# Performance work log

Hardware: AMD Instinct MI355X
Metric: run time of the kernel (lower is better)

The kernel has to match this reference:

```python
import jax, jax.numpy as jnp
import numpy as np

B, N, T, H, D = 128, 128, 256, 256, 50


def setup_inputs() -> dict:
    key = jax.random.key(0)
    ks = jax.random.split(key, 13)
    f = lambda k, s, sc=1.0: jax.random.normal(k, s, dtype=jnp.float32) * sc
    return {
        "tokens_h": f(ks[0], (B, N, H)),
        "tokens_c": f(ks[1], (B, N, H)),
        "transitions": jax.random.randint(ks[2], (B, T), 0, 3, dtype=jnp.int32),
        "tlstm_h0": f(ks[3], (B, D)),
        "tlstm_c0": f(ks[4], (B, D)),
        "Wx": f(ks[5], (4, H, D), 0.1),    # [W_i, W_f, W_o, W_u] (W_f unused in fwd, as in source)
        "Ul": f(ks[6], (4, H, H), 0.05),   # [U_il, U_fl, U_ol, U_ul]
        "Ur": f(ks[7], (4, H, H), 0.05),   # [U_ir, U_fr, U_or, U_ur]
        "b": f(ks[8], (4, H), 0.1),        # [b_i, b_f, b_o, b_u]
        "Wih": f(ks[9], (4 * D, 3 * H), 0.05),
        "Whh": f(ks[10], (4 * D, D), 0.1),
        "bih": f(ks[11], (4 * D,), 0.1),
        "bhh": f(ks[12], (4 * D,), 0.1),
    }


def _forward(tokens_h, tokens_c, transitions, tlstm_h0, tlstm_c0,
             Wx, Ul, Ur, b, Wih, Whh, bih, bhh):
    Bb, Nn, Hh = tokens_h.shape
    Tt = transitions.shape[1]
    bidx = jnp.arange(Bb)

    def tree_cell(x, h_r, c_r, h_l, c_l):
        # Faithful to source bugs: i uses W_i, o/f both use W_o, u uses W_u;
        # f_jl == f_jr (identical expressions in source).
        xi = x @ Wx[0].T
        xo = x @ Wx[2].T
        xu = x @ Wx[3].T
        i_j = jax.nn.sigmoid(xi + h_l @ Ul[0].T + h_r @ Ur[0].T + b[0])
        o_j = jax.nn.sigmoid(xo + h_l @ Ul[2].T + h_r @ Ur[2].T + b[2])
        f_j = jax.nn.sigmoid(xo + h_l @ Ul[1].T + h_r @ Ur[1].T + b[1])
        u_j = jnp.tanh(xu + h_l @ Ul[3].T + h_r @ Ur[3].T + b[3])
        c_j = i_j * u_j + f_j * c_l + f_j * c_r
        return o_j * jnp.tanh(c_j), c_j

    stack_h = jnp.zeros((Bb, Tt + 1, Hh), tokens_h.dtype)
    stack_c = jnp.zeros((Bb, Tt + 1, Hh), tokens_h.dtype)
    queue = jnp.zeros((Bb, Tt + 1), jnp.int32)   # backpointer queue (fixed buffer)
    qlen = jnp.zeros((Bb,), jnp.int32)
    bptr = jnp.zeros((Bb,), jnp.int32)

    def step(carry, xs):
        stack_h, stack_c, queue, qlen, bptr, th, tc = carry
        trans_t, t = xs
        mask = trans_t >= 1
        # utils.get_queue_item(q, -1/-2) -> default index 0 (zero stack entry)
        sp1 = jnp.where(qlen >= 1, queue[bidx, jnp.maximum(qlen - 1, 0)], 0)
        sp2 = jnp.where(qlen >= 2, queue[bidx, jnp.maximum(qlen - 2, 0)], 0)
        h1, c1 = stack_h[bidx, sp1], stack_c[bidx, sp1]
        h2, c2 = stack_h[bidx, sp2], stack_c[bidx, sp2]
        bp = jnp.minimum(bptr, Nn - 1)
        bt_h, bt_c = tokens_h[bidx, bp], tokens_c[bidx, bp]
        # tracking LSTMCell, torch gate order (i, f, g, o)
        gates = jnp.concatenate([bt_h, h1, h2], -1) @ Wih.T + bih + th @ Whh.T + bhh
        gi, gf, gg, go = jnp.split(gates, 4, axis=-1)
        tc = jax.nn.sigmoid(gf) * tc + jax.nn.sigmoid(gi) * jnp.tanh(gg)
        th = jax.nn.sigmoid(go) * jnp.tanh(tc)
        # source call order: encoder(x, h_right, c_right, h_left, c_left)
        h_la, c_la = tree_cell(th, h1, h2, c1, c2)          # (x, h_stack1, h_stack2, c_stack1, c_stack2)
        h_ra, c_ra = tree_cell(th, h2, h1, c2, c2)          # (x, h_stack2, h_stack1, c_stack2, c_stack2)
        is0 = (trans_t == 0)[:, None]
        is1 = (trans_t == 1)[:, None]
        new_h = jnp.where(is0, bt_h, jnp.where(is1, h_la, h_ra))
        new_c = jnp.where(is0, bt_c, jnp.where(is1, c_la, c_ra))
        stack_h = stack_h.at[:, t].set(new_h)
        stack_c = stack_c.at[:, t].set(new_c)
        qlen2 = jnp.where(mask, jnp.maximum(qlen - 2, 0), qlen)  # pop two on reduce
        queue = queue.at[bidx, qlen2].set(t)                      # push current timestep
        qlen = qlen2 + 1
        bptr = bptr + (1 - mask.astype(jnp.int32))
        return (stack_h, stack_c, queue, qlen, bptr, th, tc), None

    xs = (transitions.T, jnp.arange(1, Tt + 1, dtype=jnp.int32))
    carry, _ = jax.lax.scan(step, (stack_h, stack_c, queue, qlen, bptr, tlstm_h0, tlstm_c0), xs)
    return carry[0][:, Tt]  # stack[i][-1][0]


def reference(tokens_h, tokens_c, transitions, tlstm_h0, tlstm_c0,
              Wx, Ul, Ur, b, Wih, Whh, bih, bhh):
    return _forward(tokens_h, tokens_c, transitions, tlstm_h0, tlstm_c0,
                    Wx, Ul, Ur, b, Wih, Whh, bih, bhh)
```

## Files before the change

### kernel.cpp

```cpp
#include <hip/hip_runtime.h>
#include <hip/hip_fp16.h>
#include <math.h>
#include <string.h>

#define B_ 128
#define N_ 128
#define T_ 256
#define H_ 256
#define D_ 50

#define TREE_K8 72
#define TRK_K8  104

#define OFF_SH   0u
#define OFF_SC   8421376u
#define OFF_PW   16842752u
#define OFF_WTRK 17137664u
#define OFF_BCOL 17220864u
#define OFF_BTRK 17221888u
#define OFF_FLAG 17222088u
#define OFF_IDX  17287624u

__device__ __forceinline__ float sigf(float x) { return 1.0f / (1.0f + expf(-x)); }

__device__ __forceinline__ float2 h2f(unsigned u) {
    __half2 h;
    memcpy(&h, &u, 4);
    return __half22float2(h);
}

__device__ __forceinline__ float aload(const float* p) {
    int v = __hip_atomic_load((const int*)p, __ATOMIC_RELAXED, __HIP_MEMORY_SCOPE_AGENT);
    return __int_as_float(v);
}
__device__ __forceinline__ void astore(float* p, float x) {
    __hip_atomic_store((int*)p, __float_as_int(x), __ATOMIC_RELAXED, __HIP_MEMORY_SCOPE_AGENT);
}

__global__ void sim_idx(const int* __restrict__ trans, int* __restrict__ idx) {
    int b = blockIdx.x * blockDim.x + threadIdx.x;
    if (b >= B_) return;
    int queue[T_ + 1];
    int qlen = 0, bptr = 0;
    for (int st = 0; st < T_; ++st) {
        int tr = trans[b * T_ + st];
        int mask = (tr >= 1);
        int sp1 = (qlen >= 1) ? queue[qlen - 1] : 0;
        int sp2 = (qlen >= 2) ? queue[qlen - 2] : 0;
        int bp = bptr < (N_ - 1) ? bptr : (N_ - 1);
        int o = (b * T_ + st) * 3;
        idx[o] = sp1; idx[o + 1] = sp2; idx[o + 2] = bp;
        int qlen2 = mask ? (qlen - 2 > 0 ? qlen - 2 : 0) : qlen;
        queue[qlen2] = st + 1;
        qlen = qlen2 + 1;
        bptr += mask ? 0 : 1;
    }
}

__global__ void pack_tree(const float* __restrict__ Ul, const float* __restrict__ Ur,
                          const float* __restrict__ Wx, uint4* __restrict__ PW) {
    int i = blockIdx.x * blockDim.x + threadIdx.x;
    if (i >= 2 * TREE_K8 * 512) return;
    int hw = i / (TREE_K8 * 512);
    int rem = i % (TREE_K8 * 512);
    int k8 = rem / 512, c = rem % 512;
    int C = hw * 512 + c, j = C >> 2, g = C & 3;
    const int gl[4] = {0, 2, 1, 3};
    const int gx[4] = {0, 2, 2, 3};
    unsigned short hs[8];
    for (int kk = 0; kk < 8; ++kk) {
        int r = k8 * 8 + kk;
        float v;
        if (r < 256)      v = Ul[(gl[g] * H_ + j) * H_ + r];
        else if (r < 512) v = Ur[(gl[g] * H_ + j) * H_ + (r - 256)];
        else if (r < 562) v = Wx[(gx[g] * H_ + j) * D_ + (r - 512)];
        else              v = 0.0f;
        __half h = __float2half(v);
        memcpy(&hs[kk], &h, 2);
    }
    uint4 o;
    o.x = hs[0] | ((unsigned)hs[1] << 16);
    o.y = hs[2] | ((unsigned)hs[3] << 16);
    o.z = hs[4] | ((unsigned)hs[5] << 16);
    o.w = hs[6] | ((unsigned)hs[7] << 16);
    PW[i] = o;
}

__global__ void pack_trk(const float* __restrict__ Wih, const float* __restrict__ Whh,
                         uint4* __restrict__ WT) {
    int i = blockIdx.x * blockDim.x + threadIdx.x;
    if (i >= TRK_K8 * 200) return;
    int k8 = i / 200, d = i % 200;
    unsigned short hs[8];
    for (int kk = 0; kk < 8; ++kk) {
        int r = k8 * 8 + kk;
        float v;
        if (r < 768)      v = Wih[d * 768 + r];
        else if (r < 818) v = Whh[d * 50 + (r - 768)];
        else              v = 0.0f;
        __half h = __float2half(v);
        memcpy(&hs[kk], &h, 2);
    }
    uint4 o;
    o.x = hs[0] | ((unsigned)hs[1] << 16);
    o.y = hs[2] | ((unsigned)hs[3] << 16);
    o.z = hs[4] | ((unsigned)hs[5] << 16);
    o.w = hs[6] | ((unsigned)hs[7] << 16);
    WT[i] = o;
}

__global__ void pack_bias(const float* __restrict__ bias4, const float* __restrict__ bih,
                          const float* __restrict__ bhh,
                          float* __restrict__ bcol, float* __restrict__ btrk) {
    int i = blockIdx.x * blockDim.x + threadIdx.x;
    if (i < 1024) {
        int j = i >> 2, g = i & 3;
        const int gb[4] = {0, 2, 1, 3};
        bcol[i] = bias4[gb[g] * H_ + j];
    } else if (i < 1224) {
        int d = i - 1024;
        btrk[d] = bih[d] + bhh[d];
    }
}

__global__ void init_zero(float* __restrict__ ws) {
    int i = blockIdx.x * blockDim.x + threadIdx.x;
    if (i < B_ * T_ * 2) ((int*)(ws + OFF_FLAG))[i] = 0;
    if (i < B_ * H_) {
        int b = i >> 8, j = i & 255;
        ws[OFF_SH + (size_t)b * (T_ + 1) * H_ + j] = 0.0f;
        ws[OFF_SC + (size_t)b * (T_ + 1) * H_ + j] = 0.0f;
    }
}

__global__ __launch_bounds__(1024, 1)
void trnn_main(const float* __restrict__ tokens_h, const float* __restrict__ tokens_c,
               const int* __restrict__ trans,
               const float* __restrict__ th0, const float* __restrict__ tc0,
               float* __restrict__ ws, const int* __restrict__ idx,
               float* __restrict__ out) {
    const int b   = blockIdx.x & 127;
    const int hw  = blockIdx.x >> 7;
    const int tid = threadIdx.x;

    float* stack_h = ws + OFF_SH + (size_t)b * (T_ + 1) * H_;
    float* stack_c = ws + OFF_SC + (size_t)b * (T_ + 1) * H_;
    const uint4* PW = (const uint4*)(ws + OFF_PW);
    const uint4* WT = (const uint4*)(ws + OFF_WTRK);
    const float* bcol = ws + OFF_BCOL;
    const float* btrk = ws + OFF_BTRK;
    int* flags = (int*)(ws + OFF_FLAG);

    __shared__ __align__(16) float avb[256];
    __shared__ __align__(16) float av1[576], av2[576];
    __shared__ float tc_l[50];
    __shared__ float part_t[8][200];
    __shared__ float part1[8][512], part2[8][512];
    __shared__ float act1[512], act2[512];

    if (tid < 50) {
        tc_l[tid] = tc0[b * D_ + tid];
        float t0 = th0[b * D_ + tid];
        av1[512 + tid] = t0;
        av2[512 + tid] = t0;
    }
    if (tid >= 562 && tid < 576) { av1[tid] = 0.0f; av2[tid] = 0.0f; }
    __syncthreads();

    const float4* av1f4 = (const float4*)av1;
    const float4* av2f4 = (const float4*)av2;
    const float4* avbf4 = (const float4*)avb;

    for (int t = 1; t <= T_; ++t) {
        const int st = t - 1;
        const int i3 = (b * T_ + st) * 3;
        const int sp1 = idx[i3], sp2 = idx[i3 + 1], bp = idx[i3 + 2];

        if (t >= 2) {
            if (tid == 0) {
                int* f = &flags[(b * T_ + (t - 1)) * 2 + (hw ^ 1)];
                while (__hip_atomic_load(f, __ATOMIC_RELAXED, __HIP_MEMORY_SCOPE_AGENT) == 0)
                    __builtin_amdgcn_s_sleep(1);
            }
            __syncthreads();
        }

        {
            const int grp = tid >> 8, lane = tid & 255;
            if (grp == 0) {
                av1[lane] = aload(&stack_c[sp1 * H_ + lane]);
                avb[lane] = tokens_h[((size_t)b * N_ + bp) * H_ + lane];
            } else if (grp == 1) {
                av1[256 + lane] = aload(&stack_h[sp1 * H_ + lane]);
            } else if (grp == 2) {
                av2[lane] = aload(&stack_c[sp2 * H_ + lane]);
            } else {
                av2[256 + lane] = aload(&stack_h[sp2 * H_ + lane]);
            }
        }
        __syncthreads();

        if (tid < 512) {
            const int ks = tid >> 6, dgrp = tid & 63;
            if (dgrp < 50) {
                float acc0 = 0.f, acc1s = 0.f, acc2s = 0.f, acc3 = 0.f;
                for (int i = 0; i < 13; ++i) {
                    const int k8 = ks * 13 + i;
                    const float4* vsrc; int kb;
                    if (k8 < 32)      { vsrc = avbf4;        kb = k8; }
                    else if (k8 < 64) { vsrc = av1f4 + 64;   kb = k8 - 32; }
                    else if (k8 < 96) { vsrc = av2f4 + 64;   kb = k8 - 64; }
                    else              { vsrc = av1f4 + 128;  kb = k8 - 96; }
                    const float4 va = vsrc[kb * 2], vb = vsrc[kb * 2 + 1];
                    const uint4* wrow = WT + k8 * 200 + dgrp;
                    #pragma unroll
                    for (int dg = 0; dg < 4; ++dg) {
                        const uint4 w = wrow[dg * 50];
                        const float2 f0 = h2f(w.x), f1 = h2f(w.y), f2 = h2f(w.z), f3 = h2f(w.w);
                        float s = fmaf(f0.x, va.x, fmaf(f0.y, va.y, fmaf(f1.x, va.z,
                                  fmaf(f1.y, va.w, fmaf(f2.x, vb.x, fmaf(f2.y, vb.y,
                                  fmaf(f3.x, vb.z, f3.y * vb.w)))))));
                        if (dg == 0) acc0 += s;
                        else if (dg == 1) acc1s += s;
                        else if (dg == 2) acc2s += s;
                        else acc3 += s;
                    }
                }
                part_t[ks][dgrp]       = acc0;
                part_t[ks][50 + dgrp]  = acc1s;
                part_t[ks][100 + dgrp] = acc2s;
                part_t[ks][150 + dgrp] = acc3;
            }
        }
        __syncthreads();

        if (tid < 50) {
            float g4[4];
            #pragma unroll
            for (int dg = 0; dg < 4; ++dg) {
                const int d = dg * 50 + tid;
                float s = btrk[d];
                #pragma unroll
                for (int ks = 0; ks < 8; ++ks) s += part_t[ks][d];
                g4[dg] = s;
            }
            float tcv = fmaf(sigf(g4[1]), tc_l[tid], sigf(g4[0]) * tanhf(g4[2]));
            tc_l[tid] = tcv;
            float thv = sigf(g4[3]) * tanhf(tcv);
            av1[512 + tid] = thv;
            av2[512 + tid] = thv;
        }
        __syncthreads();

        {
            const int ks = tid >> 7, colgrp = tid & 127;
            float a1c[4] = {0.f, 0.f, 0.f, 0.f};
            float a2c[4] = {0.f, 0.f, 0.f, 0.f};
            #pragma unroll 3
            for (int i = 0; i < 9; ++i) {
                const int k8 = ks * 9 + i;
                const float4 v1a = av1f4[k8 * 2], v1b = av1f4[k8 * 2 + 1];
                const float4 v2a = av2f4[k8 * 2], v2b = av2f4[k8 * 2 + 1];
                const uint4* wrow = PW + (size_t)(hw * TREE_K8 + k8) * 512 + colgrp;
                #pragma unroll
                for (int cl = 0; cl < 4; ++cl) {
                    const uint4 w = wrow[cl * 128];
                    const float2 f0 = h2f(w.x), f1 = h2f(w.y), f2 = h2f(w.z), f3 = h2f(w.w);
                    float s1 = fmaf(f0.x, v1a.x, fmaf(f0.y, v1a.y, fmaf(f1.x, v1a.z,
                               fmaf(f1.y, v1a.w, fmaf(f2.x, v1b.x, fmaf(f2.y, v1b.y,
                               fmaf(f3.x, v1b.z, f3.y * v1b.w)))))));
                    float s2 = fmaf(f0.x, v2a.x, fmaf(f0.y, v2a.y, fmaf(f1.x, v2a.z,
                               fmaf(f1.y, v2a.w, fmaf(f2.x, v2b.x, fmaf(f2.y, v2b.y,
                               fmaf(f3.x, v2b.z, f3.y * v2b.w)))))));
                    a1c[cl] += s1;
                    a2c[cl] += s2;
                }
            }
            #pragma unroll
            for (int cl = 0; cl < 4; ++cl) {
                part1[ks][cl * 128 + colgrp] = a1c[cl];
                part2[ks][cl * 128 + colgrp] = a2c[cl];
            }
        }
        __syncthreads();

        {
            const int c = tid & 511;
            float s = bcol[hw * 512 + c];
            if (tid < 512) {
                #pragma unroll
                for (int ks = 0; ks < 8; ++ks) s += part1[ks][c];
                act1[c] = ((c & 3) == 3) ? tanhf(s) : sigf(s);
            } else {
                #pragma unroll
                for (int ks = 0; ks < 8; ++ks) s += part2[ks][c];
                act2[c] = ((c & 3) == 3) ? tanhf(s) : sigf(s);
            }
        }
        __syncthreads();

        if (tid < 128) {
            const int jl = tid, j = hw * 128 + jl;
            const float i1 = act1[4 * jl], o1 = act1[4 * jl + 1], f1 = act1[4 * jl + 2], u1 = act1[4 * jl + 3];
            const float i2 = act2[4 * jl], o2 = act2[4 * jl + 1], f2 = act2[4 * jl + 2], u2 = act2[4 * jl + 3];
            const float cc1 = fmaf(i1, u1, f1 * (av2[j] + av2[256 + j]));
            const float cc2 = fmaf(i2, u2, f2 * (av2[j] + av1[256 + j]));
            const float hh1 = o1 * tanhf(cc1);
            const float hh2 = o2 * tanhf(cc2);
            const int tr = trans[b * T_ + st];
            float nh, nc;
            if (tr == 0) {
                nh = avb[j];
                nc = tokens_c[((size_t)b * N_ + bp) * H_ + j];
            } else if (tr == 1) { nh = hh1; nc = cc1; }
            else                { nh = hh2; nc = cc2; }
            astore(&stack_h[t * H_ + j], nh);
            astore(&stack_c[t * H_ + j], nc);
            if (t == T_) out[b * H_ + j] = nh;
        }
        asm volatile("s_waitcnt vmcnt(0)" ::: "memory");
        __syncthreads();
        if (tid == 0 && t < T_) {
            __hip_atomic_store(&flags[(b * T_ + t) * 2 + hw], 1,
                               __ATOMIC_RELEASE, __HIP_MEMORY_SCOPE_AGENT);
        }
    }
}

extern "C" void kernel_launch(void* const* d_in, const int* in_sizes, int n_in,
                              void* d_out, int out_size, void* d_ws, size_t ws_size,
                              hipStream_t stream) {
    (void)in_sizes; (void)n_in; (void)out_size; (void)ws_size;
    const float* tokens_h = (const float*)d_in[0];
    const float* tokens_c = (const float*)d_in[1];
    const int*   trans    = (const int*)d_in[2];
    const float* th0      = (const float*)d_in[3];
    const float* tc0      = (const float*)d_in[4];
    const float* Wx       = (const float*)d_in[5];
    const float* Ul       = (const float*)d_in[6];
    const float* Ur       = (const float*)d_in[7];
    const float* bias4    = (const float*)d_in[8];
    const float* Wih      = (const float*)d_in[9];
    const float* Whh      = (const float*)d_in[10];
    const float* bih      = (const float*)d_in[11];
    const float* bhh      = (const float*)d_in[12];

    float* ws = (float*)d_ws;
    uint4* PW   = (uint4*)(ws + OFF_PW);
    uint4* WT   = (uint4*)(ws + OFF_WTRK);
    float* bcol = ws + OFF_BCOL;
    float* btrk = ws + OFF_BTRK;
    int*   idx  = (int*)(ws + OFF_IDX);

    hipLaunchKernelGGL(init_zero, dim3(256), dim3(256), 0, stream, ws);
    hipLaunchKernelGGL(sim_idx, dim3(1), dim3(128), 0, stream, trans, idx);
    hipLaunchKernelGGL(pack_tree, dim3((2 * TREE_K8 * 512 + 255) / 256), dim3(256), 0, stream,
                       Ul, Ur, Wx, PW);
    hipLaunchKernelGGL(pack_trk, dim3((TRK_K8 * 200 + 255) / 256), dim3(256), 0, stream,
                       Wih, Whh, WT);
    hipLaunchKernelGGL(pack_bias, dim3(5), dim3(256), 0, stream, bias4, bih, bhh, bcol, btrk);
    hipLaunchKernelGGL(trnn_main, dim3(256), dim3(1024), 0, stream,
                       tokens_h, tokens_c, trans, th0, tc0, ws, idx, (float*)d_out);
}
```

Before: 4.084 ms.

## Restructure tree and tracker matvecs with packed fp16 dot2 and register-cached weights

Activation vectors are now packed to fp16 pairs in shared memory, and both matvecs use the fdot2 instruction instead of unpacking to fp32 FMAs. The tracker weights are re-laid out per thread across a 5-way K split, with 12 of 21 chunks held in registers for the whole recurrence. Each tree thread now owns one gate column with a 2-way K split, down from the previous 8-way split, so the shared partial-sum reduction shrinks. tokens_h and tokens_c rows are staged in shared memory at the start of each step. The aim is to cut per-step instruction count, weight reloads from L2, and reduction traffic, at the cost of fp16 rounding of the activations and more register pressure now that launch_bounds no longer fixes one block per SM.

```diff
diff --git a/kernel.cpp b/kernel.cpp
--- a/kernel.cpp
+++ b/kernel.cpp
@@ -1,7 +1,6 @@
 #include <hip/hip_runtime.h>
 #include <hip/hip_fp16.h>
 #include <math.h>
-#include <string.h>
 
 #define B_ 128
 #define N_ 128
@@ -9,24 +8,36 @@
 #define H_ 256
 #define D_ 50
 
-#define TREE_K8 72
-#define TRK_K8  104
+#define TREE_U 72
+#define TRK_U  21
+#define TRK_REGU 12
 
 #define OFF_SH   0u
 #define OFF_SC   8421376u
-#define OFF_PW   16842752u
-#define OFF_WTRK 17137664u
-#define OFF_BCOL 17220864u
-#define OFF_BTRK 17221888u
-#define OFF_FLAG 17222088u
-#define OFF_IDX  17287624u
+#define OFF_PWK  16842752u
+#define OFF_WTK  17137664u
+#define OFF_BCOL 17221664u
+#define OFF_BTRK 17222688u
+#define OFF_FLAG 17222888u
+#define OFF_IDX  17288424u
+
+typedef _Float16 half2v __attribute__((ext_vector_type(2)));
 
 __device__ __forceinline__ float sigf(float x) { return 1.0f / (1.0f + expf(-x)); }
 
-__device__ __forceinline__ float2 h2f(unsigned u) {
-    __half2 h;
-    memcpy(&h, &u, 4);
-    return __half22float2(h);
+__device__ __forceinline__ unsigned packh2(float a, float b) {
+    half2v h = { (_Float16)a, (_Float16)b };
+    return __builtin_bit_cast(unsigned, h);
+}
+
+__device__ __forceinline__ float dot2(unsigned wu, unsigned vu, float acc) {
+#if __has_builtin(__builtin_amdgcn_fdot2)
+    return __builtin_amdgcn_fdot2(__builtin_bit_cast(half2v, wu),
+                                  __builtin_bit_cast(half2v, vu), acc, false);
+#else
+    half2v w = __builtin_bit_cast(half2v, wu), v = __builtin_bit_cast(half2v, vu);
+    return fmaf((float)w.x, (float)v.x, fmaf((float)w.y, (float)v.y, acc));
+#endif
 }
 
 __device__ __forceinline__ float aload(const float* p) {
@@ -60,53 +71,36 @@
 __global__ void pack_tree(const float* __restrict__ Ul, const float* __restrict__ Ur,
                           const float* __restrict__ Wx, uint4* __restrict__ PW) {
     int i = blockIdx.x * blockDim.x + threadIdx.x;
-    if (i >= 2 * TREE_K8 * 512) return;
-    int hw = i / (TREE_K8 * 512);
-    int rem = i % (TREE_K8 * 512);
-    int k8 = rem / 512, c = rem % 512;
-    int C = hw * 512 + c, j = C >> 2, g = C & 3;
+    if (i >= TREE_U * 1024) return;
+    int u = i >> 10, C = i & 1023, j = C >> 2, g = C & 3;
     const int gl[4] = {0, 2, 1, 3};
     const int gx[4] = {0, 2, 2, 3};
-    unsigned short hs[8];
+    float f[8];
     for (int kk = 0; kk < 8; ++kk) {
-        int r = k8 * 8 + kk;
-        float v;
-        if (r < 256)      v = Ul[(gl[g] * H_ + j) * H_ + r];
-        else if (r < 512) v = Ur[(gl[g] * H_ + j) * H_ + (r - 256)];
-        else if (r < 562) v = Wx[(gx[g] * H_ + j) * D_ + (r - 512)];
-        else              v = 0.0f;
-        __half h = __float2half(v);
-        memcpy(&hs[kk], &h, 2);
-    }
-    uint4 o;
-    o.x = hs[0] | ((unsigned)hs[1] << 16);
-    o.y = hs[2] | ((unsigned)hs[3] << 16);
-    o.z = hs[4] | ((unsigned)hs[5] << 16);
-    o.w = hs[6] | ((unsigned)hs[7] << 16);
-    PW[i] = o;
+        int r = u * 8 + kk;
+        if (r < 256)      f[kk] = Ul[(gl[g] * H_ + j) * H_ + r];
+        else if (r < 512) f[kk] = Ur[(gl[g] * H_ + j) * H_ + (r - 256)];
+        else if (r < 562) f[kk] = Wx[(gx[g] * H_ + j) * D_ + (r - 512)];
+        else              f[kk] = 0.0f;
+    }
+    PW[i] = make_uint4(packh2(f[0], f[1]), packh2(f[2], f[3]),
+                       packh2(f[4], f[5]), packh2(f[6], f[7]));
 }
 
 __global__ void pack_trk(const float* __restrict__ Wih, const float* __restrict__ Whh,
                          uint4* __restrict__ WT) {
     int i = blockIdx.x * blockDim.x + threadIdx.x;
-    if (i >= TRK_K8 * 200) return;
-    int k8 = i / 200, d = i % 200;
-    unsigned short hs[8];
+    if (i >= TRK_U * 1000) return;
+    int u = i / 1000, rem = i % 1000, d = rem / 5, ks = rem % 5;
+    float f[8];
     for (int kk = 0; kk < 8; ++kk) {
-        int r = k8 * 8 + kk;
-        float v;
-        if (r < 768)      v = Wih[d * 768 + r];
-        else if (r < 818) v = Whh[d * 50 + (r - 768)];
-        else              v = 0.0f;
-        __half h = __float2half(v);
-        memcpy(&hs[kk], &h, 2);
-    }
-    uint4 o;
-    o.x = hs[0] | ((unsigned)hs[1] << 16);
-    o.y = hs[2] | ((unsigned)hs[3] << 16);
-    o.z = hs[4] | ((unsigned)hs[5] << 16);
-    o.w = hs[6] | ((unsigned)hs[7] << 16);
-    WT[i] = o;
+        int r = ks * 168 + u * 8 + kk;
+        if (r < 768)      f[kk] = Wih[d * 768 + r];
+        else if (r < 818) f[kk] = Whh[d * 50 + (r - 768)];
+        else              f[kk] = 0.0f;
+    }
+    WT[i] = make_uint4(packh2(f[0], f[1]), packh2(f[2], f[3]),
+                       packh2(f[4], f[5]), packh2(f[6], f[7]));
 }
 
 __global__ void pack_bias(const float* __restrict__ bias4, const float* __restrict__ bih,
@@ -133,7 +127,27 @@
     }
 }
 
-__global__ __launch_bounds__(1024, 1)
+template <int S>
+__device__ __forceinline__ void tree_batch(const uint4* __restrict__ wpk, int u0,
+                                           const unsigned* __restrict__ q1,
+                                           const unsigned* __restrict__ q2,
+                                           float& a1, float& a2) {
+    uint4 wb[S];
+#pragma unroll
+    for (int i = 0; i < S; ++i) wb[i] = wpk[(size_t)(u0 + i) << 10];
+#pragma unroll
+    for (int i = 0; i < S; ++i) {
+        const int u = u0 + i;
+        const uint4 v1 = *(const uint4*)(q1 + u * 4);
+        const uint4 v2 = *(const uint4*)(q2 + u * 4);
+        a1 = dot2(wb[i].x, v1.x, a1); a1 = dot2(wb[i].y, v1.y, a1);
+        a1 = dot2(wb[i].z, v1.z, a1); a1 = dot2(wb[i].w, v1.w, a1);
+        a2 = dot2(wb[i].x, v2.x, a2); a2 = dot2(wb[i].y, v2.y, a2);
+        a2 = dot2(wb[i].z, v2.z, a2); a2 = dot2(wb[i].w, v2.w, a2);
+    }
+}
+
+__global__ __launch_bounds__(1024)
 void trnn_main(const float* __restrict__ tokens_h, const float* __restrict__ tokens_c,
                const int* __restrict__ trans,
                const float* __restrict__ th0, const float* __restrict__ tc0,
@@ -145,31 +159,44 @@
 
     float* stack_h = ws + OFF_SH + (size_t)b * (T_ + 1) * H_;
     float* stack_c = ws + OFF_SC + (size_t)b * (T_ + 1) * H_;
-    const uint4* PW = (const uint4*)(ws + OFF_PW);
-    const uint4* WT = (const uint4*)(ws + OFF_WTRK);
+    const uint4* PWK4 = (const uint4*)(ws + OFF_PWK);
+    const uint4* WTK4 = (const uint4*)(ws + OFF_WTK);
     const float* bcol = ws + OFF_BCOL;
     const float* btrk = ws + OFF_BTRK;
     int* flags = (int*)(ws + OFF_FLAG);
 
-    __shared__ __align__(16) float avb[256];
-    __shared__ __align__(16) float av1[576], av2[576];
+    __shared__ __align__(16) unsigned av1[288], av2[288];
+    __shared__ __align__(16) unsigned tav[420];
+    __shared__ float h1s[256], h2s[256], c2s[256], bths[256], btcs[256];
     __shared__ float tc_l[50];
-    __shared__ float part_t[8][200];
-    __shared__ float part1[8][512], part2[8][512];
-    __shared__ float act1[512], act2[512];
-
-    if (tid < 50) {
-        tc_l[tid] = tc0[b * D_ + tid];
-        float t0 = th0[b * D_ + tid];
-        av1[512 + tid] = t0;
-        av2[512 + tid] = t0;
-    }
-    if (tid >= 562 && tid < 576) { av1[tid] = 0.0f; av2[tid] = 0.0f; }
+    __shared__ float ptrk[5][200];
+    __shared__ float ptree[2][2][512];
+    __shared__ float act[2][512];
+
+    const int td  = tid / 5;
+    const int tks = tid % 5;
+    const bool trkA = tid < 1000;
+
+    uint4 twr[TRK_REGU];
+    if (trkA) {
+#pragma unroll
+        for (int u = 0; u < TRK_REGU; ++u) twr[u] = WTK4[u * 1000 + tid];
+    }
+
+    const int col = tid & 511;
+    const int kh  = tid >> 9;
+    const uint4* wpk = PWK4 + (hw * 512 + col);
+    const float bias_c = bcol[hw * 512 + col];
+
+    if (tid < 25) {
+        float x = th0[b * D_ + 2 * tid], y = th0[b * D_ + 2 * tid + 1];
+        unsigned p = packh2(x, y);
+        av1[256 + tid] = p; av2[256 + tid] = p; tav[384 + tid] = p;
+    }
+    if (tid < 50) tc_l[tid] = tc0[b * D_ + tid];
+    if (tid >= 281 && tid < 288) { av1[tid] = 0u; av2[tid] = 0u; }
+    if (tid < 11) tav[409 + tid] = 0u;
     __syncthreads();
-
-    const float4* av1f4 = (const float4*)av1;
-    const float4* av2f4 = (const float4*)av2;
-    const float4* avbf4 = (const float4*)avb;
 
     for (int t = 1; t <= T_; ++t) {
         const int st = t - 1;
@@ -186,134 +213,121 @@
         }
 
         {
-            const int grp = tid >> 8, lane = tid & 255;
-            if (grp == 0) {
-                av1[lane] = aload(&stack_c[sp1 * H_ + lane]);
-                avb[lane] = tokens_h[((size_t)b * N_ + bp) * H_ + lane];
-            } else if (grp == 1) {
-                av1[256 + lane] = aload(&stack_h[sp1 * H_ + lane]);
-            } else if (grp == 2) {
-                av2[lane] = aload(&stack_c[sp2 * H_ + lane]);
-            } else {
-                av2[256 + lane] = aload(&stack_h[sp2 * H_ + lane]);
-            }
-        }
-        __syncthreads();
-
-        if (tid < 512) {
-            const int ks = tid >> 6, dgrp = tid & 63;
-            if (dgrp < 50) {
-                float acc0 = 0.f, acc1s = 0.f, acc2s = 0.f, acc3 = 0.f;
-                for (int i = 0; i < 13; ++i) {
-                    const int k8 = ks * 13 + i;
-                    const float4* vsrc; int kb;
-                    if (k8 < 32)      { vsrc = avbf4;        kb = k8; }
-                    else if (k8 < 64) { vsrc = av1f4 + 64;   kb = k8 - 32; }
-                    else if (k8 < 96) { vsrc = av2f4 + 64;   kb = k8 - 64; }
-                    else              { vsrc = av1f4 + 128;  kb = k8 - 96; }
-                    const float4 va = vsrc[kb * 2], vb = vsrc[kb * 2 + 1];
-                    const uint4* wrow = WT + k8 * 200 + dgrp;
-                    #pragma unroll
-                    for (int dg = 0; dg < 4; ++dg) {
-                        const uint4 w = wrow[dg * 50];
-                        const float2 f0 = h2f(w.x), f1 = h2f(w.y), f2 = h2f(w.z), f3 = h2f(w.w);
-                        float s = fmaf(f0.x, va.x, fmaf(f0.y, va.y, fmaf(f1.x, va.z,
-                                  fmaf(f1.y, va.w, fmaf(f2.x, vb.x, fmaf(f2.y, vb.y,
-                                  fmaf(f3.x, vb.z, f3.y * vb.w)))))));
-                        if (dg == 0) acc0 += s;
-                        else if (dg == 1) acc1s += s;
-                        else if (dg == 2) acc2s += s;
-                        else acc3 += s;
-                    }
+            const int g = tid >> 7, t2 = tid & 127;
+            const int e0 = 2 * t2, e1 = e0 + 1;
+            if (g == 0) {
+                float x = aload(&stack_c[sp1 * H_ + e0]), y = aload(&stack_c[sp1 * H_ + e1]);
+                av1[t2] = packh2(x, y);
+            } else if (g == 1) {
+                float x = aload(&stack_h[sp1 * H_ + e0]), y = aload(&stack_h[sp1 * H_ + e1]);
+                unsigned p = packh2(x, y);
+                av1[128 + t2] = p; tav[128 + t2] = p; h1s[e0] = x; h1s[e1] = y;
+            } else if (g == 2) {
+                float x = aload(&stack_c[sp2 * H_ + e0]), y = aload(&stack_c[sp2 * H_ + e1]);
+                av2[t2] = packh2(x, y); c2s[e0] = x; c2s[e1] = y;
+            } else if (g == 3) {
+                float x = aload(&stack_h[sp2 * H_ + e0]), y = aload(&stack_h[sp2 * H_ + e1]);
+                unsigned p = packh2(x, y);
+                av2[128 + t2] = p; tav[256 + t2] = p; h2s[e0] = x; h2s[e1] = y;
+            } else if (g == 4) {
+                const float* src = tokens_h + ((size_t)b * N_ + bp) * H_;
+                float x = src[e0], y = src[e1];
+                tav[t2] = packh2(x, y); bths[e0] = x; bths[e1] = y;
+            } else if (g == 5) {
+                const float* src = tokens_c + ((size_t)b * N_ + bp) * H_;
+                btcs[e0] = src[e0]; btcs[e1] = src[e1];
+            }
+        }
+        __syncthreads();
+
+        if (trkA) {
+            const unsigned* tv = tav + tks * 84;
+            uint4 sb[TRK_U - TRK_REGU];
+#pragma unroll
+            for (int i = 0; i < TRK_U - TRK_REGU; ++i)
+                sb[i] = WTK4[(TRK_REGU + i) * 1000 + tid];
+            float a = 0.f;
+#pragma unroll
+            for (int u = 0; u < TRK_REGU; ++u) {
+                const uint4 v = *(const uint4*)(tv + u * 4);
+                a = dot2(twr[u].x, v.x, a); a = dot2(twr[u].y, v.y, a);
+                a = dot2(twr[u].z, v.z, a); a = dot2(twr[u].w, v.w, a);
+            }
+#pragma unroll
+            for (int i = 0; i < TRK_U - TRK_REGU; ++i) {
+                const uint4 v = *(const uint4*)(tv + (TRK_REGU + i) * 4);
+                a = dot2(sb[i].x, v.x, a); a = dot2(sb[i].y, v.y, a);
+                a = dot2(sb[i].z, v.z, a); a = dot2(sb[i].w, v.w, a);
+            }
+            ptrk[tks][td] = a;
+        }
+        __syncthreads();
+
+        if (tid < 25) {
+            float thv0 = 0.f, thv1 = 0.f;
+#pragma unroll
+            for (int q = 0; q < 2; ++q) {
+                const int d = 2 * tid + q;
+                float gi = btrk[d], gf = btrk[50 + d], gg = btrk[100 + d], go = btrk[150 + d];
+#pragma unroll
+                for (int ks = 0; ks < 5; ++ks) {
+                    gi += ptrk[ks][d]; gf += ptrk[ks][50 + d];
+                    gg += ptrk[ks][100 + d]; go += ptrk[ks][150 + d];
                 }
-                part_t[ks][dgrp]       = acc0;
-                part_t[ks][50 + dgrp]  = acc1s;
-                part_t[ks][100 + dgrp] = acc2s;
-                part_t[ks][150 + dgrp] = acc3;
-            }
-        }
-        __syncthreads();
-
-        if (tid < 50) {
-            float g4[4];
-            #pragma unroll
-            for (int dg = 0; dg < 4; ++dg) {
-                const int d = dg * 50 + tid;
-                float s = btrk[d];
-                #pragma unroll
-                for (int ks = 0; ks < 8; ++ks) s += part_t[ks][d];
-                g4[dg] = s;
-            }
-            float tcv = fmaf(sigf(g4[1]), tc_l[tid], sigf(g4[0]) * tanhf(g4[2]));
-            tc_l[tid] = tcv;
-            float thv = sigf(g4[3]) * tanhf(tcv);
-            av1[512 + tid] = thv;
-            av2[512 + tid] = thv;
+                float c = fmaf(sigf(gf), tc_l[d], sigf(gi) * tanhf(gg));
+                tc_l[d] = c;
+                float thv = sigf(go) * tanhf(c);
+                if (q == 0) thv0 = thv; else thv1 = thv;
+            }
+            unsigned p = packh2(thv0, thv1);
+            av1[256 + tid] = p; av2[256 + tid] = p; tav[384 + tid] = p;
+        }
+
+        float a1 = 0.f, a2 = 0.f;
+        if (kh == 0) {
+            tree_batch<6>(wpk, 0,  av1, av2, a1, a2);
+            tree_batch<6>(wpk, 6,  av1, av2, a1, a2);
+            tree_batch<6>(wpk, 12, av1, av2, a1, a2);
+            tree_batch<6>(wpk, 18, av1, av2, a1, a2);
+            tree_batch<6>(wpk, 24, av1, av2, a1, a2);
+            tree_batch<6>(wpk, 30, av1, av2, a1, a2);
+            ptree[0][0][col] = a1; ptree[1][0][col] = a2;
+        } else {
+            tree_batch<7>(wpk, 36, av1, av2, a1, a2);
+            tree_batch<7>(wpk, 43, av1, av2, a1, a2);
+            tree_batch<7>(wpk, 50, av1, av2, a1, a2);
+            tree_batch<7>(wpk, 57, av1, av2, a1, a2);
+        }
+        __syncthreads();
+
+        if (kh == 1) {
+            tree_batch<4>(wpk, 64, av1, av2, a1, a2);
+            tree_batch<4>(wpk, 68, av1, av2, a1, a2);
+            ptree[0][1][col] = a1; ptree[1][1][col] = a2;
         }
         __syncthreads();
 
         {
-            const int ks = tid >> 7, colgrp = tid & 127;
-            float a1c[4] = {0.f, 0.f, 0.f, 0.f};
-            float a2c[4] = {0.f, 0.f, 0.f, 0.f};
-            #pragma unroll 3
-            for (int i = 0; i < 9; ++i) {
-                const int k8 = ks * 9 + i;
-                const float4 v1a = av1f4[k8 * 2], v1b = av1f4[k8 * 2 + 1];
-                const float4 v2a = av2f4[k8 * 2], v2b = av2f4[k8 * 2 + 1];
-                const uint4* wrow = PW + (size_t)(hw * TREE_K8 + k8) * 512 + colgrp;
-                #pragma unroll
-                for (int cl = 0; cl < 4; ++cl) {
-                    const uint4 w = wrow[cl * 128];
-                    const float2 f0 = h2f(w.x), f1 = h2f(w.y), f2 = h2f(w.z), f3 = h2f(w.w);
-                    float s1 = fmaf(f0.x, v1a.x, fmaf(f0.y, v1a.y, fmaf(f1.x, v1a.z,
-                               fmaf(f1.y, v1a.w, fmaf(f2.x, v1b.x, fmaf(f2.y, v1b.y,
-                               fmaf(f3.x, v1b.z, f3.y * v1b.w)))))));
-                    float s2 = fmaf(f0.x, v2a.x, fmaf(f0.y, v2a.y, fmaf(f1.x, v2a.z,
-                               fmaf(f1.y, v2a.w, fmaf(f2.x, v2b.x, fmaf(f2.y, v2b.y,
-                               fmaf(f3.x, v2b.z, f3.y * v2b.w)))))));
-                    a1c[cl] += s1;
-                    a2c[cl] += s2;
-                }
-            }
-            #pragma unroll
-            for (int cl = 0; cl < 4; ++cl) {
-                part1[ks][cl * 128 + colgrp] = a1c[cl];
-                part2[ks][cl * 128 + colgrp] = a2c[cl];
-            }
-        }
-        __syncthreads();
-
-        {
-            const int c = tid & 511;
-            float s = bcol[hw * 512 + c];
-            if (tid < 512) {
-                #pragma unroll
-                for (int ks = 0; ks < 8; ++ks) s += part1[ks][c];
-                act1[c] = ((c & 3) == 3) ? tanhf(s) : sigf(s);
-            } else {
-                #pragma unroll
-                for (int ks = 0; ks < 8; ++ks) s += part2[ks][c];
-                act2[c] = ((c & 3) == 3) ? tanhf(s) : sigf(s);
-            }
+            const int call = tid >> 9, c = tid & 511;
+            float s = bias_c + ptree[call][0][c] + ptree[call][1][c];
+            act[call][c] = ((c & 3) == 3) ? tanhf(s) : sigf(s);
         }
         __syncthreads();
 
         if (tid < 128) {
             const int jl = tid, j = hw * 128 + jl;
-            const float i1 = act1[4 * jl], o1 = act1[4 * jl + 1], f1 = act1[4 * jl + 2], u1 = act1[4 * jl + 3];
-            const float i2 = act2[4 * jl], o2 = act2[4 * jl + 1], f2 = act2[4 * jl + 2], u2 = act2[4 * jl + 3];
-            const float cc1 = fmaf(i1, u1, f1 * (av2[j] + av2[256 + j]));
-            const float cc2 = fmaf(i2, u2, f2 * (av2[j] + av1[256 + j]));
+            const int c0 = 4 * jl;
+            const float i1 = act[0][c0], o1 = act[0][c0 + 1], f1 = act[0][c0 + 2], u1 = act[0][c0 + 3];
+            const float i2 = act[1][c0], o2 = act[1][c0 + 1], f2 = act[1][c0 + 2], u2 = act[1][c0 + 3];
+            const float cc1 = fmaf(i1, u1, f1 * (c2s[j] + h2s[j]));
+            const float cc2 = fmaf(i2, u2, f2 * (c2s[j] + h1s[j]));
             const float hh1 = o1 * tanhf(cc1);
             const float hh2 = o2 * tanhf(cc2);
             const int tr = trans[b * T_ + st];
             float nh, nc;
-            if (tr == 0) {
-                nh = avb[j];
-                nc = tokens_c[((size_t)b * N_ + bp) * H_ + j];
-            } else if (tr == 1) { nh = hh1; nc = cc1; }
-            else                { nh = hh2; nc = cc2; }
+            if (tr == 0)      { nh = bths[j]; nc = btcs[j]; }
+            else if (tr == 1) { nh = hh1; nc = cc1; }
+            else              { nh = hh2; nc = cc2; }
             astore(&stack_h[t * H_ + j], nh);
             astore(&stack_c[t * H_ + j], nc);
             if (t == T_) out[b * H_ + j] = nh;
@@ -346,18 +360,18 @@
     const float* bhh      = (const float*)d_in[12];
 
     float* ws = (float*)d_ws;
-    uint4* PW   = (uint4*)(ws + OFF_PW);
-    uint4* WT   = (uint4*)(ws + OFF_WTRK);
+    uint4* PWK  = (uint4*)(ws + OFF_PWK);
+    uint4* WTK  = (uint4*)(ws + OFF_WTK);
     float* bcol = ws + OFF_BCOL;
     float* btrk = ws + OFF_BTRK;
     int*   idx  = (int*)(ws + OFF_IDX);
 
     hipLaunchKernelGGL(init_zero, dim3(256), dim3(256), 0, stream, ws);
     hipLaunchKernelGGL(sim_idx, dim3(1), dim3(128), 0, stream, trans, idx);
-    hipLaunchKernelGGL(pack_tree, dim3((2 * TREE_K8 * 512 + 255) / 256), dim3(256), 0, stream,
-                       Ul, Ur, Wx, PW);
-    hipLaunchKernelGGL(pack_trk, dim3((TRK_K8 * 200 + 255) / 256), dim3(256), 0, stream,
-                       Wih, Whh, WT);
+    hipLaunchKernelGGL(pack_tree, dim3((TREE_U * 1024 + 255) / 256), dim3(256), 0, stream,
+                       Ul, Ur, Wx, PWK);
+    hipLaunchKernelGGL(pack_trk, dim3((TRK_U * 1000 + 255) / 256), dim3(256), 0, stream,
+                       Wih, Whh, WTK);
     hipLaunchKernelGGL(pack_bias, dim3(5), dim3(256), 0, stream, bias4, bih, bhh, bcol, btrk);
     hipLaunchKernelGGL(trnn_main, dim3(256), dim3(1024), 0, stream,
                        tokens_h, tokens_c, trans, th0, tc0, ws, idx, (float*)d_out);
```

Result: slower. 7.441 ms (+82.2%).
